# Kernel tuning notes

Hardware: AMD Instinct MI355X
Metric: run time of the kernel (lower is better)

The kernel has to match this reference:

```python
import jax, jax.numpy as jnp
import numpy as np

VOCAB = 50257
EMB = 512


def setup_inputs() -> dict:
    key = jax.random.key(0)
    k1, k2, k3 = jax.random.split(key, 3)
    input_token_ids = jax.random.randint(k1, (8, 4096), 0, VOCAB, dtype=jnp.int64 if jax.config.jax_enable_x64 else jnp.int32)
    W = jax.random.normal(k2, (EMB, VOCAB), dtype=jnp.float32)  # nn.Linear(vocab, emb).weight
    b = jax.random.normal(k3, (EMB,), dtype=jnp.float32)        # nn.Linear bias
    return {"input_token_ids": input_token_ids, "W": W, "b": b}


def reference(input_token_ids, W, b):
    # one_hot(ids, V) @ W.T + b  ==  W.T[ids] + b   (exact same math, gather form)
    scale = jnp.asarray(EMB, W.dtype) ** 0.5
    emb = jnp.take(W.T, input_token_ids, axis=0)  # [B, S, EMB]
    return (emb + b) * scale
```

## Files before the change

### kernel.cpp

```cpp
#include <hip/hip_runtime.h>
#include <hip/hip_bf16.h>


constexpr int VOCAB = 50257;
constexpr int EMB   = 512;
constexpr int NTOK  = 8 * 4096;
constexpr float SCALE = 22.62741699796952f;

constexpr int VB  = 32;
constexpr int NB  = (VOCAB + VB - 1) / VB;
constexpr int CAP = 128;
constexpr int ECH = 256;


__global__ __launch_bounds__(256) void init_counts(int* __restrict__ counts) {
    int i = blockIdx.x * 256 + threadIdx.x;
    if (i < NB + 1) counts[i] = 0;
}

__global__ __launch_bounds__(256) void build_buckets(
    const int* __restrict__ ids,
    int* __restrict__ counts,
    int* __restrict__ olist,
    int* __restrict__ buckets)
{
    int t = blockIdx.x * 256 + threadIdx.x;
    int id = ids[t];
    int bkt = id >> 5;
    int slot = atomicAdd(&counts[bkt], 1);
    if (slot < CAP) {
        buckets[bkt * CAP + slot] = (t << 5) | (id & 31);
    } else {
        int o = atomicAdd(&counts[NB], 1);
        olist[o] = t;
    }
}

__global__ __launch_bounds__(256) void scatter_main(
    const float* __restrict__ W,
    const float* __restrict__ bias,
    const int*   __restrict__ counts,
    const int*   __restrict__ buckets,
    float*       __restrict__ out)
{
    __shared__ float tile[VB][ECH + 1];
    __shared__ int   toks[CAP];
    __shared__ int   s_cnt;

    int b   = blockIdx.x;
    int v0  = b * VB;
    int tid = threadIdx.x;

    if (tid == 0) s_cnt = counts[b];
    if (tid < CAP) toks[tid] = buckets[b * CAP + tid];
    __syncthreads();
    int cnt = min(s_cnt, CAP);
    if (cnt == 0) return;

    int tx   = tid & 31;
    int ty   = tid >> 5;
    int sub  = tid >> 6;
    int lane = tid & 63;

    int v = v0 + tx;
    bool vok = v < VOCAB;

    for (int chunk = 0; chunk < EMB / ECH; ++chunk) {
        int e0 = chunk * ECH;
        #pragma unroll
        for (int p = 0; p < ECH / 8; ++p) {
            int el = p * 8 + ty;
            int e  = e0 + el;
            float val = 0.0f;
            if (vok) val = (W[(size_t)e * VOCAB + v] + bias[e]) * SCALE;
            tile[tx][el] = val;
        }
        __syncthreads();
        for (int i = sub; i < cnt; i += 4) {
            int pk = toks[i];
            int t  = pk >> 5;
            int vl = pk & 31;
            float* op = out + (size_t)t * EMB + e0 + lane;
            #pragma unroll
            for (int m = 0; m < ECH / 64; ++m)
                op[m * 64] = tile[vl][lane + m * 64];
        }
        __syncthreads();
    }
}

__global__ __launch_bounds__(256) void overflow_fix(
    const int*   __restrict__ counts,
    const int*   __restrict__ olist,
    const int*   __restrict__ ids,
    const float* __restrict__ W,
    const float* __restrict__ bias,
    float*       __restrict__ out)
{
    int n    = counts[NB];
    int wid  = (blockIdx.x * 256 + threadIdx.x) >> 6;
    int lane = threadIdx.x & 63;
    int nw   = (gridDim.x * 256) >> 6;
    for (int w = wid; w < n; w += nw) {
        int t  = olist[w];
        int id = ids[t];
        #pragma unroll
        for (int m = 0; m < 8; ++m) {
            int e = lane + m * 64;
            out[(size_t)t * EMB + e] = (W[(size_t)e * VOCAB + id] + bias[e]) * SCALE;
        }
    }
}

__global__ __launch_bounds__(256) void embed_gather(
    const int*   __restrict__ ids,
    const float* __restrict__ W,
    const float* __restrict__ b,
    float*       __restrict__ out)
{
    int idx4 = blockIdx.x * blockDim.x + threadIdx.x;
    int t    = idx4 >> 7;
    int e    = (idx4 & 127) << 2;
    int id = ids[t];
    float4 bb = *reinterpret_cast<const float4*>(b + e);
    const float* wcol = W + (size_t)id;
    float4 o;
    o.x = (wcol[(size_t)(e + 0) * VOCAB] + bb.x) * SCALE;
    o.y = (wcol[(size_t)(e + 1) * VOCAB] + bb.y) * SCALE;
    o.z = (wcol[(size_t)(e + 2) * VOCAB] + bb.z) * SCALE;
    o.w = (wcol[(size_t)(e + 3) * VOCAB] + bb.w) * SCALE;
    *reinterpret_cast<float4*>(out + (size_t)idx4 * 4) = o;
}

extern "C" void kernel_launch(void* const* d_in, const int* in_sizes, int n_in,
                              void* d_out, int out_size, void* d_ws, size_t ws_size,
                              hipStream_t stream)
{
    const int*   ids  = (const int*)  d_in[0];
    const float* W    = (const float*)d_in[1];
    const float* bias = (const float*)d_in[2];
    float*       out  = (float*)d_out;

    const size_t ws_ints_needed = (size_t)NB + 1 + NTOK + (size_t)NB * CAP;

    if (ws_size >= ws_ints_needed * sizeof(int)) {
        int* counts  = (int*)d_ws;
        int* olist   = counts + NB + 1;
        int* buckets = olist + NTOK;

        init_counts<<<(NB + 1 + 255) / 256, 256, 0, stream>>>(counts);
        build_buckets<<<NTOK / 256, 256, 0, stream>>>(ids, counts, olist, buckets);
        scatter_main<<<NB, 256, 0, stream>>>(W, bias, counts, buckets, out);
        overflow_fix<<<32, 256, 0, stream>>>(counts, olist, ids, W, bias, out);
    } else {
        constexpr int total4 = NTOK * EMB / 4;
        embed_gather<<<total4 / 256, 256, 0, stream>>>(ids, W, bias, out);
    }
}
```

Measured before the change: 200.4 us.

## Load W tiles directly into LDS and write float4 outputs with deferred bias

Replaces the register-staged W tile load with global_load_lds direct-to-LDS transfers, using a padded 65-stride layout that holds two embedding rows per 64-lane wave. The bias add and scale move from tile construction to the output phase, and each lane now writes a float4 of four consecutive embedding values instead of four strided scalar stores. The aim is to cut VGPR traffic and the number of store instructions. In exchange, bias is reloaded for every token, an unused bias_scaled parameter is passed as nullptr, and out-of-range vocab lanes now load W[0] instead of writing zero.

```diff
diff --git a/kernel.cpp b/kernel.cpp
--- a/kernel.cpp
+++ b/kernel.cpp
@@ -39,11 +39,12 @@
 __global__ __launch_bounds__(256) void scatter_main(
     const float* __restrict__ W,
     const float* __restrict__ bias,
+    const float* __restrict__ bias_scaled,
     const int*   __restrict__ counts,
     const int*   __restrict__ buckets,
     float*       __restrict__ out)
 {
-    __shared__ float tile[VB][ECH + 1];
+    __shared__ float tile[(ECH / 2) * 65];
     __shared__ int   toks[CAP];
     __shared__ int   s_cnt;
 
@@ -57,33 +58,45 @@
     int cnt = min(s_cnt, CAP);
     if (cnt == 0) return;
 
+    int lane = tid & 63;
+    int w    = tid >> 6;
     int tx   = tid & 31;
-    int ty   = tid >> 5;
-    int sub  = tid >> 6;
-    int lane = tid & 63;
 
     int v = v0 + tx;
     bool vok = v < VOCAB;
 
     for (int chunk = 0; chunk < EMB / ECH; ++chunk) {
         int e0 = chunk * ECH;
+
         #pragma unroll
         for (int p = 0; p < ECH / 8; ++p) {
-            int el = p * 8 + ty;
-            int e  = e0 + el;
-            float val = 0.0f;
-            if (vok) val = (W[(size_t)e * VOCAB + v] + bias[e]) * SCALE;
-            tile[tx][el] = val;
+            int el = p * 8 + 2 * w + (lane >> 5);
+            size_t gidx = (size_t)(e0 + el) * VOCAB + v;
+            if (!vok) gidx = 0;
+            const float* gp = W + gidx;
+            float* lp = &tile[(p * 4 + w) * 65];
+            __builtin_amdgcn_global_load_lds(
+                (const __attribute__((address_space(1))) void*)gp,
+                (__attribute__((address_space(3))) void*)lp, 4, 0, 0);
         }
         __syncthreads();
-        for (int i = sub; i < cnt; i += 4) {
+
+        for (int i = w; i < cnt; i += 4) {
             int pk = toks[i];
             int t  = pk >> 5;
             int vl = pk & 31;
-            float* op = out + (size_t)t * EMB + e0 + lane;
-            #pragma unroll
-            for (int m = 0; m < ECH / 64; ++m)
-                op[m * 64] = tile[vl][lane + m * 64];
+            int g0 = 2 * lane;
+            float4 o;
+            o.x = tile[g0 * 65 + vl];
+            o.y = tile[g0 * 65 + 32 + vl];
+            o.z = tile[(g0 + 1) * 65 + vl];
+            o.w = tile[(g0 + 1) * 65 + 32 + vl];
+            int e = e0 + 4 * lane;
+            o.x = (o.x + bias[e + 0]) * SCALE;
+            o.y = (o.y + bias[e + 1]) * SCALE;
+            o.z = (o.z + bias[e + 2]) * SCALE;
+            o.w = (o.w + bias[e + 3]) * SCALE;
+            *reinterpret_cast<float4*>(out + (size_t)t * EMB + e) = o;
         }
         __syncthreads();
     }
@@ -101,8 +114,8 @@
     int wid  = (blockIdx.x * 256 + threadIdx.x) >> 6;
     int lane = threadIdx.x & 63;
     int nw   = (gridDim.x * 256) >> 6;
-    for (int w = wid; w < n; w += nw) {
-        int t  = olist[w];
+    for (int ww = wid; ww < n; ww += nw) {
+        int t  = olist[ww];
         int id = ids[t];
         #pragma unroll
         for (int m = 0; m < 8; ++m) {
@@ -150,7 +163,7 @@
 
         init_counts<<<(NB + 1 + 255) / 256, 256, 0, stream>>>(counts);
         build_buckets<<<NTOK / 256, 256, 0, stream>>>(ids, counts, olist, buckets);
-        scatter_main<<<NB, 256, 0, stream>>>(W, bias, counts, buckets, out);
+        scatter_main<<<NB, 256, 0, stream>>>(W, bias, nullptr, counts, buckets, out);
         overflow_fix<<<32, 256, 0, stream>>>(counts, olist, ids, W, bias, out);
     } else {
         constexpr int total4 = NTOK * EMB / 4;
```

Result: faster. 189.6 us (-5.4%).

## Split scatter per wavefront with async global-to-LDS double-buffered tile loads

Applied to the files above, without the earlier changes.

Rewrites scatter_main so each wavefront independently handles one vocab bucket and a 128-wide slice of the embedding dimension. W columns are loaded straight into LDS with global_load_lds into two 64-row buffers. The first buffer's writes overlap the second buffer's loads through partial vmcnt waits, and block-level barriers are removed. Bias and scale are now applied at write time, and token lists are broadcast with readlane. This depends on manual waitcnt counting and on the LDS layout matching the per-lane load addressing, which is fragile.

```diff
diff --git a/kernel.cpp b/kernel.cpp
--- a/kernel.cpp
+++ b/kernel.cpp
@@ -10,7 +10,7 @@
 constexpr int VB  = 32;
 constexpr int NB  = (VOCAB + VB - 1) / VB;
 constexpr int CAP = 128;
-constexpr int ECH = 256;
+constexpr int CH  = 64;
 
 
 __global__ __launch_bounds__(256) void init_counts(int* __restrict__ counts) {
@@ -43,49 +43,70 @@
     const int*   __restrict__ buckets,
     float*       __restrict__ out)
 {
-    __shared__ float tile[VB][ECH + 1];
-    __shared__ int   toks[CAP];
-    __shared__ int   s_cnt;
+    __shared__ float tile[4][2][(CH / 2) * 65];
 
-    int b   = blockIdx.x;
-    int v0  = b * VB;
-    int tid = threadIdx.x;
+    int tid  = threadIdx.x;
+    int w    = tid >> 6;
+    int lane = tid & 63;
 
-    if (tid == 0) s_cnt = counts[b];
-    if (tid < CAP) toks[tid] = buckets[b * CAP + tid];
-    __syncthreads();
-    int cnt = min(s_cnt, CAP);
+    int u = blockIdx.x * 4 + w;
+    int b = u >> 2;
+    int q = u & 3;
+    int e_base = q * 128;
+
+    int cnt = counts[b];
+    cnt = min(cnt, CAP);
     if (cnt == 0) return;
 
-    int tx   = tid & 31;
-    int ty   = tid >> 5;
-    int sub  = tid >> 6;
-    int lane = tid & 63;
+    const int* bk = buckets + b * CAP;
+    int pk0 = bk[lane];
+    int pk1 = bk[64 + lane];
 
-    int v = v0 + tx;
-    bool vok = v < VOCAB;
+    int vg = b * VB + (lane & 31);
+    size_t vcl = (vg < VOCAB) ? (size_t)vg : (size_t)(VOCAB - 1);
 
-    for (int chunk = 0; chunk < EMB / ECH; ++chunk) {
-        int e0 = chunk * ECH;
+    float* buf0 = &tile[w][0][0];
+    float* buf1 = &tile[w][1][0];
+
+    {
+        const float* gp0 = W + (size_t)(e_base + (lane >> 5)) * VOCAB + vcl;
         #pragma unroll
-        for (int p = 0; p < ECH / 8; ++p) {
-            int el = p * 8 + ty;
-            int e  = e0 + el;
-            float val = 0.0f;
-            if (vok) val = (W[(size_t)e * VOCAB + v] + bias[e]) * SCALE;
-            tile[tx][el] = val;
-        }
-        __syncthreads();
-        for (int i = sub; i < cnt; i += 4) {
-            int pk = toks[i];
+        for (int g = 0; g < CH / 2; ++g)
+            __builtin_amdgcn_global_load_lds(
+                (const __attribute__((address_space(1))) void*)(gp0 + (size_t)(2 * g) * VOCAB),
+                (__attribute__((address_space(3))) void*)(buf0 + g * 65), 4, 0, 0);
+        const float* gp1 = W + (size_t)(e_base + CH + (lane >> 5)) * VOCAB + vcl;
+        #pragma unroll
+        for (int g = 0; g < CH / 2; ++g)
+            __builtin_amdgcn_global_load_lds(
+                (const __attribute__((address_space(1))) void*)(gp1 + (size_t)(2 * g) * VOCAB),
+                (__attribute__((address_space(3))) void*)(buf1 + g * 65), 4, 0, 0);
+    }
+
+    int laddr = (lane >> 1) * 65 + (lane & 1) * 32;
+
+    asm volatile("s_waitcnt vmcnt(32)" ::: "memory");
+    {
+        int e = e_base + lane;
+        float bb = bias[e];
+        for (int i = 0; i < cnt; ++i) {
+            int pk = __builtin_amdgcn_readlane(i < 64 ? pk0 : pk1, i & 63);
             int t  = pk >> 5;
             int vl = pk & 31;
-            float* op = out + (size_t)t * EMB + e0 + lane;
-            #pragma unroll
-            for (int m = 0; m < ECH / 64; ++m)
-                op[m * 64] = tile[vl][lane + m * 64];
+            out[(size_t)t * EMB + e] = (buf0[laddr + vl] + bb) * SCALE;
         }
-        __syncthreads();
+    }
+
+    asm volatile("s_waitcnt vmcnt(0)" ::: "memory");
+    {
+        int e = e_base + CH + lane;
+        float bb = bias[e];
+        for (int i = 0; i < cnt; ++i) {
+            int pk = __builtin_amdgcn_readlane(i < 64 ? pk0 : pk1, i & 63);
+            int t  = pk >> 5;
+            int vl = pk & 31;
+            out[(size_t)t * EMB + e] = (buf1[laddr + vl] + bb) * SCALE;
+        }
     }
 }
 
@@ -101,8 +122,8 @@
     int wid  = (blockIdx.x * 256 + threadIdx.x) >> 6;
     int lane = threadIdx.x & 63;
     int nw   = (gridDim.x * 256) >> 6;
-    for (int w = wid; w < n; w += nw) {
-        int t  = olist[w];
+    for (int ww = wid; ww < n; ww += nw) {
+        int t  = olist[ww];
         int id = ids[t];
         #pragma unroll
         for (int m = 0; m < 8; ++m) {
```

New measurement: 196.4 us. 1.02x faster.
